# Performance work log

Measured on AMD Instinct MI355X. Metric: run time of the kernel, lower is better.

## Reference

```python
import jax, jax.numpy as jnp
import numpy as np

TEMPERATURE = 0.5  # init kwarg: temperature
EPS = 1e-8         # torch CosineSimilarity eps


def setup_inputs() -> dict:
    key = jax.random.key(0)
    k1, k2 = jax.random.split(key)
    B, D = 2048, 256
    return {
        "z_i": jax.random.normal(k1, (B, D), dtype=jnp.float32),
        "z_j": jax.random.normal(k2, (B, D), dtype=jnp.float32),
    }


def reference(z_i, z_j):
    # NT-Xent (SimCLR) loss, world_size = 1.
    B = z_i.shape[0]
    N = 2 * B
    z = jnp.concatenate([z_i, z_j], axis=0)                       # [N, D]
    # Cosine similarity = normalized dot product (fused normalize + matmul,
    # avoiding the torch broadcast NxNxD intermediate).
    zn = z / jnp.clip(jnp.linalg.norm(z, axis=1, keepdims=True), EPS)
    sim = (zn @ zn.T) / TEMPERATURE                               # [N, N]
    # Positive pair similarity for each row: diag offsets +B and -B.
    pos = jnp.concatenate([jnp.diagonal(sim, offset=B),
                           jnp.diagonal(sim, offset=-B)], axis=0)  # [N]
    # CrossEntropy with label 0 over logits [pos, negatives] equals
    # -pos + logsumexp over {pos} U negatives = all off-diagonal entries,
    # since the mask removes exactly the diagonal and the positive pair
    # (which is re-added as `pos`). Mask diagonal with -inf.
    neg_inf = jnp.finfo(sim.dtype).min
    sim_masked = jnp.where(jnp.eye(N, dtype=bool), neg_inf, sim)
    lse = jax.scipy.special.logsumexp(sim_masked, axis=1)          # [N]
    # reduction='sum' then / N  ->  mean over rows
    loss = jnp.sum(lse - pos) / N
    return loss
```

## Files before the change

kernel.cpp:

```cpp
#include <hip/hip_runtime.h>


#define NROWS 4096
#define DDIM 256
#define BHALF 2048
#define TILE 128
#define BK 64
#define LDP 72
#define NCB 32
#define INV_T 2.0f

typedef short bf16x8 __attribute__((ext_vector_type(8)));
typedef float f32x4 __attribute__((ext_vector_type(4)));

__device__ inline unsigned short f2bf(float f) {
    union { float f; unsigned u; } c; c.f = f;
    unsigned u = c.u + 0x7fffu + ((c.u >> 16) & 1u);
    return (unsigned short)(u >> 16);
}

__global__ __launch_bounds__(256) void k_normalize(
    const float* __restrict__ zi, const float* __restrict__ zj,
    unsigned short* __restrict__ zn, float* __restrict__ out) {
    if (blockIdx.x == 0 && threadIdx.x == 0) out[0] = 0.f;
    const int wave = threadIdx.x >> 6, lane = threadIdx.x & 63;
    const int row = blockIdx.x * 4 + wave;
    const float* src = (row < BHALF) ? (zi + row * DDIM)
                                     : (zj + (row - BHALF) * DDIM);
    const float4 v = ((const float4*)src)[lane];
    float ss = v.x * v.x + v.y * v.y + v.z * v.z + v.w * v.w;
    #pragma unroll
    for (int m = 1; m < 64; m <<= 1) ss += __shfl_xor(ss, m);
    const float scale = 1.0f / fmaxf(sqrtf(ss), 1e-8f);
    ushort4 o;
    o.x = f2bf(v.x * scale); o.y = f2bf(v.y * scale);
    o.z = f2bf(v.z * scale); o.w = f2bf(v.w * scale);
    ((ushort4*)(zn + row * DDIM))[lane] = o;
}

__global__ __launch_bounds__(256) void k_simlse(
    const unsigned short* __restrict__ zn,
    float* __restrict__ partial,
    float* __restrict__ posv) {
    __shared__ unsigned short As[TILE * LDP];
    __shared__ unsigned short Bs[TILE * LDP];
    __shared__ float pscratch[TILE];
    __shared__ float cscratch[TILE];

    int t = blockIdx.x, bx = 0, rem = NCB;
    while (t >= rem) { t -= rem; ++bx; --rem; }
    const int by = bx + t;

    const int tid = threadIdx.x;
    const int wave = tid >> 6, lane = tid & 63;
    const int quad = lane >> 4, l15 = lane & 15;
    const int wr = wave >> 1, wc = wave & 1;
    const int rowBase = bx * TILE;
    const int colBase = by * TILE;

    f32x4 acc[4][4] = {};

    #pragma unroll
    for (int kb = 0; kb < DDIM / BK; ++kb) {
        __syncthreads();
        #pragma unroll
        for (int i = 0; i < 4; ++i) {
            const int flat = tid + i * 256;
            const int r = flat >> 3, c = flat & 7;
            *(bf16x8*)&As[r * LDP + c * 8] =
                *(const bf16x8*)&zn[(rowBase + r) * DDIM + kb * BK + c * 8];
            *(bf16x8*)&Bs[r * LDP + c * 8] =
                *(const bf16x8*)&zn[(colBase + r) * DDIM + kb * BK + c * 8];
        }
        __syncthreads();
        #pragma unroll
        for (int s = 0; s < 2; ++s) {
            bf16x8 af[4], bf[4];
            #pragma unroll
            for (int mt = 0; mt < 4; ++mt)
                af[mt] = *(const bf16x8*)&As[(wr * 64 + mt * 16 + l15) * LDP + s * 32 + quad * 8];
            #pragma unroll
            for (int nt = 0; nt < 4; ++nt)
                bf[nt] = *(const bf16x8*)&Bs[(wc * 64 + nt * 16 + l15) * LDP + s * 32 + quad * 8];
            #pragma unroll
            for (int mt = 0; mt < 4; ++mt)
                #pragma unroll
                for (int nt = 0; nt < 4; ++nt)
                    acc[mt][nt] = __builtin_amdgcn_mfma_f32_16x16x32_bf16(
                        af[mt], bf[nt], acc[mt][nt], 0, 0, 0);
        }
    }

    float rsum[4][4];
    float csum[4] = {};
    #pragma unroll
    for (int mt = 0; mt < 4; ++mt) {
        #pragma unroll
        for (int r = 0; r < 4; ++r) {
            const int grow = rowBase + wr * 64 + mt * 16 + quad * 4 + r;
            float s = 0.f;
            #pragma unroll
            for (int nt = 0; nt < 4; ++nt) {
                const int gcol = colBase + wc * 64 + nt * 16 + l15;
                const float simv = acc[mt][nt][r] * INV_T;
                const float e = (gcol != grow) ? __expf(simv) : 0.f;
                s += e;
                csum[nt] += e;
                if (gcol == grow + BHALF) {
                    posv[grow] = simv;
                    posv[gcol] = simv;
                }
            }
            s += __shfl_xor(s, 1); s += __shfl_xor(s, 2);
            s += __shfl_xor(s, 4); s += __shfl_xor(s, 8);
            rsum[mt][r] = s;
        }
    }
    #pragma unroll
    for (int nt = 0; nt < 4; ++nt) {
        csum[nt] += __shfl_xor(csum[nt], 16);
        csum[nt] += __shfl_xor(csum[nt], 32);
    }

    __syncthreads();
    if (wc == 0 && l15 == 0) {
        #pragma unroll
        for (int mt = 0; mt < 4; ++mt)
            #pragma unroll
            for (int r = 0; r < 4; ++r)
                pscratch[wr * 64 + mt * 16 + quad * 4 + r] = rsum[mt][r];
    }
    if (wr == 0 && quad == 0) {
        #pragma unroll
        for (int nt = 0; nt < 4; ++nt)
            cscratch[wc * 64 + nt * 16 + l15] = csum[nt];
    }
    __syncthreads();
    if (wc == 1 && l15 == 0) {
        #pragma unroll
        for (int mt = 0; mt < 4; ++mt)
            #pragma unroll
            for (int r = 0; r < 4; ++r) {
                const int lr = wr * 64 + mt * 16 + quad * 4 + r;
                partial[by * NROWS + rowBase + lr] = rsum[mt][r] + pscratch[lr];
            }
    }
    if (bx != by && wr == 1 && quad == 0) {
        #pragma unroll
        for (int nt = 0; nt < 4; ++nt) {
            const int lc = wc * 64 + nt * 16 + l15;
            partial[bx * NROWS + colBase + lc] = csum[nt] + cscratch[lc];
        }
    }
}

__global__ __launch_bounds__(256) void k_rowlse(
    const float* __restrict__ partial, const float* __restrict__ posv,
    float* __restrict__ out) {
    __shared__ float red[4];
    const int tid = threadIdx.x;
    const int row = blockIdx.x * 256 + tid;
    float s = 0.f;
    #pragma unroll
    for (int p = 0; p < NCB; ++p) s += partial[p * NROWS + row];
    float v = __logf(s) - posv[row];
    #pragma unroll
    for (int m = 1; m < 64; m <<= 1) v += __shfl_xor(v, m);
    if ((tid & 63) == 0) red[tid >> 6] = v;
    __syncthreads();
    if (tid == 0)
        atomicAdd(out, (red[0] + red[1] + red[2] + red[3]) * (1.0f / (float)NROWS));
}

extern "C" void kernel_launch(void* const* d_in, const int* in_sizes, int n_in,
                              void* d_out, int out_size, void* d_ws, size_t ws_size,
                              hipStream_t stream) {
    const float* zi = (const float*)d_in[0];
    const float* zj = (const float*)d_in[1];
    float* out = (float*)d_out;

    unsigned short* zn = (unsigned short*)d_ws;
    float* partial = (float*)((char*)d_ws + NROWS * DDIM * 2);
    float* posv = partial + NCB * NROWS;

    k_normalize<<<NROWS / 4, 256, 0, stream>>>(zi, zj, zn, out);
    k_simlse<<<NCB * (NCB + 1) / 2, 256, 0, stream>>>(zn, partial, posv);
    k_rowlse<<<16, 256, 0, stream>>>(partial, posv, out);
}
```

Before: 78.24 us.

## Shrink similarity tiles to 64x64 to launch more blocks across CUs

Changes the triangular tiling of the similarity matrix from 128x128 to 64x64 tiles. The grid grows from 528 to 2080 blocks, and each wave now owns a 16x64 strip with four MFMA accumulators. The row/column partial-sum reduction is restructured to match, and the partial buffer doubles to 64 column blocks. The aim is better occupancy and load balance on the many-CU GPU. The cost is less data reuse per tile, more global loads and a larger final reduction in k_rowlse.

```diff
diff --git a/kernel.cpp b/kernel.cpp
--- a/kernel.cpp
+++ b/kernel.cpp
@@ -4,10 +4,11 @@
 #define NROWS 4096
 #define DDIM 256
 #define BHALF 2048
-#define TILE 128
+#define TILE 64
 #define BK 64
 #define LDP 72
-#define NCB 32
+#define NCB 64
+#define NBLK (NCB * (NCB + 1) / 2)
 #define INV_T 2.0f
 
 typedef short bf16x8 __attribute__((ext_vector_type(8)));
@@ -44,8 +45,7 @@
     float* __restrict__ posv) {
     __shared__ unsigned short As[TILE * LDP];
     __shared__ unsigned short Bs[TILE * LDP];
-    __shared__ float pscratch[TILE];
-    __shared__ float cscratch[TILE];
+    __shared__ float cscratch[4 * TILE];
 
     int t = blockIdx.x, bx = 0, rem = NCB;
     while (t >= rem) { t -= rem; ++bx; --rem; }
@@ -54,17 +54,16 @@
     const int tid = threadIdx.x;
     const int wave = tid >> 6, lane = tid & 63;
     const int quad = lane >> 4, l15 = lane & 15;
-    const int wr = wave >> 1, wc = wave & 1;
     const int rowBase = bx * TILE;
     const int colBase = by * TILE;
 
-    f32x4 acc[4][4] = {};
+    f32x4 acc[4] = {};
 
     #pragma unroll
     for (int kb = 0; kb < DDIM / BK; ++kb) {
         __syncthreads();
         #pragma unroll
-        for (int i = 0; i < 4; ++i) {
+        for (int i = 0; i < 2; ++i) {
             const int flat = tid + i * 256;
             const int r = flat >> 3, c = flat & 7;
             *(bf16x8*)&As[r * LDP + c * 8] =
@@ -75,46 +74,41 @@
         __syncthreads();
         #pragma unroll
         for (int s = 0; s < 2; ++s) {
-            bf16x8 af[4], bf[4];
-            #pragma unroll
-            for (int mt = 0; mt < 4; ++mt)
-                af[mt] = *(const bf16x8*)&As[(wr * 64 + mt * 16 + l15) * LDP + s * 32 + quad * 8];
+            const bf16x8 af =
+                *(const bf16x8*)&As[(wave * 16 + l15) * LDP + s * 32 + quad * 8];
+            bf16x8 bf[4];
             #pragma unroll
             for (int nt = 0; nt < 4; ++nt)
-                bf[nt] = *(const bf16x8*)&Bs[(wc * 64 + nt * 16 + l15) * LDP + s * 32 + quad * 8];
+                bf[nt] = *(const bf16x8*)&Bs[(nt * 16 + l15) * LDP + s * 32 + quad * 8];
             #pragma unroll
-            for (int mt = 0; mt < 4; ++mt)
-                #pragma unroll
-                for (int nt = 0; nt < 4; ++nt)
-                    acc[mt][nt] = __builtin_amdgcn_mfma_f32_16x16x32_bf16(
-                        af[mt], bf[nt], acc[mt][nt], 0, 0, 0);
+            for (int nt = 0; nt < 4; ++nt)
+                acc[nt] = __builtin_amdgcn_mfma_f32_16x16x32_bf16(
+                    af, bf[nt], acc[nt], 0, 0, 0);
         }
     }
 
-    float rsum[4][4];
+    const int wrow = rowBase + wave * 16;
+    float rsum[4];
     float csum[4] = {};
     #pragma unroll
-    for (int mt = 0; mt < 4; ++mt) {
+    for (int r = 0; r < 4; ++r) {
+        const int grow = wrow + quad * 4 + r;
+        float s = 0.f;
         #pragma unroll
-        for (int r = 0; r < 4; ++r) {
-            const int grow = rowBase + wr * 64 + mt * 16 + quad * 4 + r;
-            float s = 0.f;
-            #pragma unroll
-            for (int nt = 0; nt < 4; ++nt) {
-                const int gcol = colBase + wc * 64 + nt * 16 + l15;
-                const float simv = acc[mt][nt][r] * INV_T;
-                const float e = (gcol != grow) ? __expf(simv) : 0.f;
-                s += e;
-                csum[nt] += e;
-                if (gcol == grow + BHALF) {
-                    posv[grow] = simv;
-                    posv[gcol] = simv;
-                }
+        for (int nt = 0; nt < 4; ++nt) {
+            const int gcol = colBase + nt * 16 + l15;
+            const float simv = acc[nt][r] * INV_T;
+            const float e = (gcol != grow) ? __expf(simv) : 0.f;
+            s += e;
+            csum[nt] += e;
+            if (gcol == grow + BHALF) {
+                posv[grow] = simv;
+                posv[gcol] = simv;
             }
-            s += __shfl_xor(s, 1); s += __shfl_xor(s, 2);
-            s += __shfl_xor(s, 4); s += __shfl_xor(s, 8);
-            rsum[mt][r] = s;
         }
+        s += __shfl_xor(s, 1); s += __shfl_xor(s, 2);
+        s += __shfl_xor(s, 4); s += __shfl_xor(s, 8);
+        rsum[r] = s;
     }
     #pragma unroll
     for (int nt = 0; nt < 4; ++nt) {
@@ -122,35 +116,21 @@
         csum[nt] += __shfl_xor(csum[nt], 32);
     }
 
-    __syncthreads();
-    if (wc == 0 && l15 == 0) {
+    if (l15 == 0) {
         #pragma unroll
-        for (int mt = 0; mt < 4; ++mt)
-            #pragma unroll
-            for (int r = 0; r < 4; ++r)
-                pscratch[wr * 64 + mt * 16 + quad * 4 + r] = rsum[mt][r];
+        for (int r = 0; r < 4; ++r)
+            partial[by * NROWS + wrow + quad * 4 + r] = rsum[r];
     }
-    if (wr == 0 && quad == 0) {
+    if (quad == 0) {
         #pragma unroll
         for (int nt = 0; nt < 4; ++nt)
-            cscratch[wc * 64 + nt * 16 + l15] = csum[nt];
+            cscratch[wave * TILE + nt * 16 + l15] = csum[nt];
     }
     __syncthreads();
-    if (wc == 1 && l15 == 0) {
-        #pragma unroll
-        for (int mt = 0; mt < 4; ++mt)
-            #pragma unroll
-            for (int r = 0; r < 4; ++r) {
-                const int lr = wr * 64 + mt * 16 + quad * 4 + r;
-                partial[by * NROWS + rowBase + lr] = rsum[mt][r] + pscratch[lr];
-            }
-    }
-    if (bx != by && wr == 1 && quad == 0) {
-        #pragma unroll
-        for (int nt = 0; nt < 4; ++nt) {
-            const int lc = wc * 64 + nt * 16 + l15;
-            partial[bx * NROWS + colBase + lc] = csum[nt] + cscratch[lc];
-        }
+    if (bx != by && tid < TILE) {
+        const float cs = cscratch[tid] + cscratch[TILE + tid]
+                       + cscratch[2 * TILE + tid] + cscratch[3 * TILE + tid];
+        partial[bx * NROWS + colBase + tid] = cs;
     }
 }
 
@@ -184,6 +164,6 @@
     float* posv = partial + NCB * NROWS;
 
     k_normalize<<<NROWS / 4, 256, 0, stream>>>(zi, zj, zn, out);
-    k_simlse<<<NCB * (NCB + 1) / 2, 256, 0, stream>>>(zn, partial, posv);
+    k_simlse<<<NBLK, 256, 0, stream>>>(zn, partial, posv);
     k_rowlse<<<16, 256, 0, stream>>>(partial, posv, out);
 }
```

Result: slower. 94.37 us (+20.6%).
